# Performance work log

Hardware: AMD Instinct MI355X
Metric: run time of the kernel (lower is better)

The kernel has to match this reference:

```python
import jax, jax.numpy as jnp
import numpy as np

# dims: N sentences, L tokens each, M=2 memory slots/sentence, D hidden, H heads
N, L, M, D, H, FF, V, P, LAYERS = 4, 256, 2, 768, 12, 3072, 32000, 1024, 4
DH = D // H


def setup_inputs() -> dict:
    key = jax.random.key(0)
    ks = jax.random.split(key, 20)
    s = 0.02
    inp = {
        'input_ids': jax.random.randint(ks[0], (N, L), 0, V),
        'memory': jax.random.normal(ks[1], (N, M, D), jnp.float32),
        'emb_table': jax.random.normal(ks[2], (V, D), jnp.float32) * s,
        'pos_table': jax.random.normal(ks[3], (P + 2, D), jnp.float32) * s,
        'Wq': jax.random.normal(ks[4], (LAYERS, D, D), jnp.float32) * s,
        'bq': jnp.zeros((LAYERS, D), jnp.float32),
        'Wk': jax.random.normal(ks[5], (LAYERS, D, D), jnp.float32) * s,
        'bk': jnp.zeros((LAYERS, D), jnp.float32),
        'Wv': jax.random.normal(ks[6], (LAYERS, D, D), jnp.float32) * s,
        'bv': jnp.zeros((LAYERS, D), jnp.float32),
        'W1': jax.random.normal(ks[7], (LAYERS, D, FF), jnp.float32) * s,
        'b1': jnp.zeros((LAYERS, FF), jnp.float32),
        'W2': jax.random.normal(ks[8], (LAYERS, FF, D), jnp.float32) * s,
        'b2': jnp.zeros((LAYERS, D), jnp.float32),
        'g1': jnp.ones((LAYERS, D), jnp.float32),
        'be1': jnp.zeros((LAYERS, D), jnp.float32),
        'g2': jnp.ones((LAYERS, D), jnp.float32),
        'be2': jnp.zeros((LAYERS, D), jnp.float32),
    }
    return inp


def _layer_norm(x, g, b):
    mu = jnp.mean(x, axis=-1, keepdims=True)
    var = jnp.mean((x - mu) ** 2, axis=-1, keepdims=True)
    return (x - mu) / jnp.sqrt(var + 1e-5) * g + b


def _encoder(input_ids, memory, emb_table, pos_table, Wq, bq, Wk, bk, Wv, bv,
             W1, b1, W2, b2, g1, be1, g2, be2):
    base = N * M            # token rows start here in the packed input
    T = base + N * L        # total rows (memory rows + token rows)
    Kk = M + L              # keys per query (own memory + own tokens)

    # position embeddings: memory rows get pos (p % M); tokens get id_pos + M
    mem_pos = jnp.tile(jnp.arange(M), N)                    # (N*M,)
    mem = memory.reshape(N * M, D) + pos_table[mem_pos]
    fwd_pos = jnp.tile(jnp.arange(L) + M, N)                # (N*L,)
    tok = emb_table[input_ids.reshape(-1)] + pos_table[fwd_pos]
    x = jnp.concatenate([mem, tok], axis=0)                 # (T, D)

    # per-sentence key set: its M memory rows then its L token rows
    key_pos = jnp.concatenate([
        jnp.arange(N)[:, None] * M + jnp.arange(M)[None, :],
        base + jnp.arange(N)[:, None] * L + jnp.arange(L)[None, :],
    ], axis=1)                                              # (N, Kk)
    sent = jnp.concatenate([jnp.repeat(jnp.arange(N), M),
                            jnp.repeat(jnp.arange(N), L)])  # (T,)
    gidx = key_pos[sent]                                    # (T, Kk)
    # equal-length sentences => the additive mask built by the torch code is
    # all zeros (key_len == max_key_len for every row), so it is omitted.

    scale = 1.0 / np.sqrt(DH)
    for i in range(LAYERS):
        # K/V are linear row-wise, so project once on all rows then gather
        # (identical math to projecting the gathered tgt, without T-fold GEMM)
        q = (x @ Wq[i] + bq[i]).reshape(T, H, DH)
        kf = (x @ Wk[i] + bk[i]).reshape(T, H, DH)
        vf = (x @ Wv[i] + bv[i]).reshape(T, H, DH)
        kg = kf[gidx]                                       # (T, Kk, H, DH)
        vg = vf[gidx]
        scores = jnp.einsum('thd,tkhd->thk', q, kg) * scale
        probs = jax.nn.softmax(scores, axis=-1)
        ctx = jnp.einsum('thk,tkhd->thd', probs, vg).reshape(T, D)
        x = _layer_norm(x + ctx, g1[i], be1[i])
        h = jax.nn.gelu(x @ W1[i] + b1[i], approximate=False)
        x = _layer_norm(x + h @ W2[i] + b2[i], g2[i], be2[i])

    ret = key_pos[:, M:]                                    # (N, L) token rows
    return x[ret]                                           # (N, L, D)


def reference(input_ids, memory, emb_table, pos_table, Wq, bq, Wk, bk, Wv, bv,
              W1, b1, W2, b2, g1, be1, g2, be2):
    return _encoder(input_ids, memory, emb_table, pos_table, Wq, bq, Wk, bk,
                    Wv, bv, W1, b1, W2, b2, g1, be1, g2, be2)
```

## Files before the change

kernel.cpp:

```cpp
#include <hip/hip_runtime.h>
#include <hip/hip_bf16.h>
#include <math.h>

#define N_      4
#define L_      256
#define M_      2
#define D_      768
#define H_      12
#define FF_     3072
#define DH_     64
#define LAYERS_ 4
#define BASE_   8
#define T_      1032
#define TP_     1088
#define KK_     258
#define QS_     2304
#define PS_     264

typedef __bf16 bf16x8 __attribute__((ext_vector_type(8)));
typedef float  f32x4  __attribute__((ext_vector_type(4)));

__device__ __forceinline__ void async_load16(const __hip_bfloat16* g, __hip_bfloat16* l) {
  __builtin_amdgcn_global_load_lds(
      (const __attribute__((address_space(1))) unsigned int*)g,
      (__attribute__((address_space(3))) unsigned int*)l, 16, 0, 0);
}

__global__ __launch_bounds__(256) void transpose_cast_kernel(
    const float* __restrict__ src, __hip_bfloat16* __restrict__ dst, int K, int N) {
  __shared__ float tile[32][33];
  const int k0 = blockIdx.y * 32, n0 = blockIdx.x * 32;
  const int r = threadIdx.x >> 5, c = threadIdx.x & 31;
  #pragma unroll
  for (int i = 0; i < 4; ++i)
    tile[r + i * 8][c] = src[(size_t)(k0 + r + i * 8) * N + n0 + c];
  __syncthreads();
  #pragma unroll
  for (int i = 0; i < 4; ++i)
    dst[(size_t)(n0 + r + i * 8) * K + k0 + c] = __float2bfloat16(tile[c][r + i * 8]);
}

__global__ __launch_bounds__(256) void pack_bias_kernel(
    const float* __restrict__ bq, const float* __restrict__ bk,
    const float* __restrict__ bv, float* __restrict__ out) {
  int i = blockIdx.x * 256 + threadIdx.x;
  int l = i / QS_, j = i - l * QS_;
  float v;
  if (j < D_)            v = bq[l * D_ + j];
  else if (j < 2 * D_)   v = bk[l * D_ + (j - D_)];
  else                   v = bv[l * D_ + (j - 2 * D_)];
  out[i] = v;
}

__global__ __launch_bounds__(256) void embed_kernel(
    const int* __restrict__ ids, const float* __restrict__ memory,
    const float* __restrict__ emb, const float* __restrict__ pos,
    float* __restrict__ x, __hip_bfloat16* __restrict__ xb) {
  int row = blockIdx.x;
  const float *src, *p;
  if (row < BASE_) {
    src = memory + (long long)row * D_;
    p   = pos + (row & 1) * D_;
  } else {
    int i = row - BASE_;
    int tok = ids[i];
    src = emb + (long long)tok * D_;
    p   = pos + (M_ + (i & (L_ - 1))) * D_;
  }
  for (int d = threadIdx.x; d < D_; d += 256) {
    float v = src[d] + p[d];
    x[(long long)row * D_ + d]  = v;
    xb[(long long)row * D_ + d] = __float2bfloat16(v);
  }
}

template <int ACT, int WF32, int WBF16, int WVT>
__global__ __launch_bounds__(256) void gemm_mfma(
    const __hip_bfloat16* __restrict__ A,
    const __hip_bfloat16* __restrict__ Bt,
    const float* __restrict__ bias,
    float* __restrict__ C,
    __hip_bfloat16* __restrict__ Cb,
    __hip_bfloat16* __restrict__ vt,
    int N, int K) {
  __shared__ __align__(16) __hip_bfloat16 As[4][64][32];
  __shared__ __align__(16) __hip_bfloat16 Bs[4][64][32];
  const int tid  = threadIdx.x;
  const int lane = tid & 63, wid = tid >> 6;
  const int ln   = lane & 15, qd = lane >> 4;
  const int wm   = wid >> 1, wn = wid & 1;

  const size_t arow = (size_t)(blockIdx.y * 64 + wid * 16 + (lane >> 2)) * K + (lane & 3) * 8;
  const size_t brow = (size_t)(blockIdx.x * 64 + wid * 16 + (lane >> 2)) * K + (lane & 3) * 8;

  f32x4 acc[2][2] = {};
  for (int k0 = 0; k0 < K; k0 += 128) {
    #pragma unroll
    for (int s = 0; s < 4; ++s) {
      async_load16(A  + arow + k0 + s * 32, &As[s][wid * 16][0]);
      async_load16(Bt + brow + k0 + s * 32, &Bs[s][wid * 16][0]);
    }
    __syncthreads();
    #pragma unroll
    for (int s = 0; s < 4; ++s) {
      bf16x8 a0 = *(const bf16x8*)&As[s][wm * 32 + ln][qd * 8];
      bf16x8 a1 = *(const bf16x8*)&As[s][wm * 32 + 16 + ln][qd * 8];
      bf16x8 b0 = *(const bf16x8*)&Bs[s][wn * 32 + ln][qd * 8];
      bf16x8 b1 = *(const bf16x8*)&Bs[s][wn * 32 + 16 + ln][qd * 8];
      acc[0][0] = __builtin_amdgcn_mfma_f32_16x16x32_bf16(a0, b0, acc[0][0], 0, 0, 0);
      acc[0][1] = __builtin_amdgcn_mfma_f32_16x16x32_bf16(a0, b1, acc[0][1], 0, 0, 0);
      acc[1][0] = __builtin_amdgcn_mfma_f32_16x16x32_bf16(a1, b0, acc[1][0], 0, 0, 0);
      acc[1][1] = __builtin_amdgcn_mfma_f32_16x16x32_bf16(a1, b1, acc[1][1], 0, 0, 0);
    }
    __syncthreads();
  }
  #pragma unroll
  for (int mt = 0; mt < 2; ++mt) {
    #pragma unroll
    for (int nt = 0; nt < 2; ++nt) {
      const int col = blockIdx.x * 64 + wn * 32 + nt * 16 + ln;
      const float bv = bias[col];
      #pragma unroll
      for (int i = 0; i < 4; ++i) {
        const int row = blockIdx.y * 64 + wm * 32 + mt * 16 + qd * 4 + i;
        float v = acc[mt][nt][i] + bv;
        if (ACT) v = 0.5f * v * (1.f + erff(v * 0.70710678118654752f));
        if (WF32)  C[(size_t)row * N + col]  = v;
        if (WVT) {
          if (col < 2 * D_) Cb[(size_t)row * N + col] = __float2bfloat16(v);
          else              vt[(size_t)(col - 2 * D_) * TP_ + row] = __float2bfloat16(v);
        } else if (WBF16) {
          Cb[(size_t)row * N + col] = __float2bfloat16(v);
        }
      }
    }
  }
}

__global__ __launch_bounds__(256) void attn_mfma(
    const __hip_bfloat16* __restrict__ qkv,
    const __hip_bfloat16* __restrict__ vtb,
    float* __restrict__ ctx) {
  __shared__ __align__(16) __hip_bfloat16 Ps[64][PS_];
  const int qt = blockIdx.x, h = blockIdx.y, b = blockIdx.z;
  const int tid = threadIdx.x;
  const int w = tid >> 6, lane = tid & 63, ln = lane & 15, qd = lane >> 4;

  bf16x8 aq0, aq1;
  {
    int j = qt * 64 + w * 16 + ln;
    int tok = (j < 256) ? (BASE_ + b * L_ + j)
            : ((j < KK_) ? (b * M_ + (j - 256)) : (b * M_));
    const __hip_bfloat16* qp = qkv + (size_t)tok * QS_ + h * DH_ + qd * 8;
    aq0 = *(const bf16x8*)qp;
    aq1 = *(const bf16x8*)(qp + 32);
  }

  f32x4 sa[17];
  #pragma unroll
  for (int nt = 0; nt < 17; ++nt) sa[nt] = (f32x4){0.f, 0.f, 0.f, 0.f};
  #pragma unroll
  for (int nt = 0; nt < 17; ++nt) {
    int key = nt * 16 + ln;
    int ktok = (key < 256) ? (BASE_ + b * L_ + key)
             : ((key < KK_) ? (b * M_ + (key - 256)) : (b * M_));
    const __hip_bfloat16* kp = qkv + (size_t)ktok * QS_ + D_ + h * DH_ + qd * 8;
    bf16x8 b0 = *(const bf16x8*)kp;
    bf16x8 b1 = *(const bf16x8*)(kp + 32);
    sa[nt] = __builtin_amdgcn_mfma_f32_16x16x32_bf16(aq0, b0, sa[nt], 0, 0, 0);
    sa[nt] = __builtin_amdgcn_mfma_f32_16x16x32_bf16(aq1, b1, sa[nt], 0, 0, 0);
  }

  #pragma unroll
  for (int i = 0; i < 4; ++i) {
    float v[17];
    #pragma unroll
    for (int nt = 0; nt < 17; ++nt) v[nt] = sa[nt][i] * 0.125f;
    float mx = -1e30f;
    #pragma unroll
    for (int nt = 0; nt < 16; ++nt) mx = fmaxf(mx, v[nt]);
    if (ln < 2) mx = fmaxf(mx, v[16]);
    #pragma unroll
    for (int m = 1; m < 16; m <<= 1) mx = fmaxf(mx, __shfl_xor(mx, m));
    float sum = 0.f;
    #pragma unroll
    for (int nt = 0; nt < 17; ++nt) {
      float e = (nt == 16 && ln >= 2) ? 0.f : __expf(v[nt] - mx);
      v[nt] = e;
      sum += e;
    }
    #pragma unroll
    for (int m = 1; m < 16; m <<= 1) sum += __shfl_xor(sum, m);
    float is = 1.f / sum;
    const int row = w * 16 + qd * 4 + i;
    #pragma unroll
    for (int nt = 0; nt < 17; ++nt)
      if (nt < 16 || ln < 2)
        Ps[row][nt * 16 + ln] = __float2bfloat16(v[nt] * is);
  }

  f32x4 oa[4] = {};
  #pragma unroll
  for (int k0 = 0; k0 < 8; ++k0) {
    bf16x8 ap = *(const bf16x8*)&Ps[w * 16 + ln][k0 * 32 + qd * 8];
    #pragma unroll
    for (int nt = 0; nt < 4; ++nt) {
      const __hip_bfloat16* vp = vtb + (size_t)(h * DH_ + nt * 16 + ln) * TP_
                               + BASE_ + b * L_ + k0 * 32 + qd * 8;
      bf16x8 bv = *(const bf16x8*)vp;
      oa[nt] = __builtin_amdgcn_mfma_f32_16x16x32_bf16(ap, bv, oa[nt], 0, 0, 0);
    }
  }
  {
    float p0[4], p1[4];
    #pragma unroll
    for (int i = 0; i < 4; ++i) {
      p0[i] = __bfloat162float(Ps[w * 16 + qd * 4 + i][256]);
      p1[i] = __bfloat162float(Ps[w * 16 + qd * 4 + i][257]);
    }
    #pragma unroll
    for (int nt = 0; nt < 4; ++nt) {
      const __hip_bfloat16* vp = vtb + (size_t)(h * DH_ + nt * 16 + ln) * TP_ + b * M_;
      float v0 = __bfloat162float(vp[0]);
      float v1 = __bfloat162float(vp[1]);
      #pragma unroll
      for (int i = 0; i < 4; ++i) oa[nt][i] += p0[i] * v0 + p1[i] * v1;
    }
  }

  #pragma unroll
  for (int i = 0; i < 4; ++i) {
    int j = qt * 64 + w * 16 + qd * 4 + i;
    if (j < KK_) {
      int tok = (j < 256) ? (BASE_ + b * L_ + j) : (b * M_ + (j - 256));
      #pragma unroll
      for (int nt = 0; nt < 4; ++nt)
        ctx[(size_t)tok * D_ + h * DH_ + nt * 16 + ln] = oa[nt][i];
    }
  }
}

__global__ __launch_bounds__(256) void add_ln_kernel(
    float* __restrict__ x, const float* __restrict__ delta,
    const float* __restrict__ g, const float* __restrict__ b,
    __hip_bfloat16* __restrict__ xb) {
  __shared__ float sred[4];
  __shared__ float sbc;
  const int t = blockIdx.x, tid = threadIdx.x;
  float y[3];
  float s = 0.f;
  #pragma unroll
  for (int i = 0; i < 3; ++i) {
    int d = tid + i * 256;
    y[i] = x[(long long)t * D_ + d] + delta[(long long)t * D_ + d];
    s += y[i];
  }
  #pragma unroll
  for (int o = 32; o > 0; o >>= 1) s += __shfl_down(s, o);
  if ((tid & 63) == 0) sred[tid >> 6] = s;
  __syncthreads();
  if (tid == 0) sbc = (sred[0] + sred[1] + sred[2] + sred[3]) * (1.f / D_);
  __syncthreads();
  const float mu = sbc;
  __syncthreads();
  float vs = 0.f;
  #pragma unroll
  for (int i = 0; i < 3; ++i) { float d = y[i] - mu; vs += d * d; }
  #pragma unroll
  for (int o = 32; o > 0; o >>= 1) vs += __shfl_down(vs, o);
  if ((tid & 63) == 0) sred[tid >> 6] = vs;
  __syncthreads();
  if (tid == 0) sbc = (sred[0] + sred[1] + sred[2] + sred[3]) * (1.f / D_);
  __syncthreads();
  const float inv = rsqrtf(sbc + 1e-5f);
  #pragma unroll
  for (int i = 0; i < 3; ++i) {
    int d = tid + i * 256;
    float v = (y[i] - mu) * inv * g[d] + b[d];
    x[(long long)t * D_ + d]  = v;
    xb[(long long)t * D_ + d] = __float2bfloat16(v);
  }
}

__global__ __launch_bounds__(256) void out_copy_kernel(
    const float* __restrict__ x, float* __restrict__ out, int n) {
  int i = blockIdx.x * 256 + threadIdx.x;
  if (i < n) out[i] = x[BASE_ * D_ + i];
}

extern "C" void kernel_launch(void* const* d_in, const int* in_sizes, int n_in,
                              void* d_out, int out_size, void* d_ws, size_t ws_size,
                              hipStream_t stream) {
  const int*   ids    = (const int*)  d_in[0];
  const float* memory = (const float*)d_in[1];
  const float* emb    = (const float*)d_in[2];
  const float* pos    = (const float*)d_in[3];
  const float* Wq     = (const float*)d_in[4];
  const float* bq     = (const float*)d_in[5];
  const float* Wk     = (const float*)d_in[6];
  const float* bk     = (const float*)d_in[7];
  const float* Wv     = (const float*)d_in[8];
  const float* bv     = (const float*)d_in[9];
  const float* W1     = (const float*)d_in[10];
  const float* b1     = (const float*)d_in[11];
  const float* W2     = (const float*)d_in[12];
  const float* b2     = (const float*)d_in[13];
  const float* g1     = (const float*)d_in[14];
  const float* be1    = (const float*)d_in[15];
  const float* g2     = (const float*)d_in[16];
  const float* be2    = (const float*)d_in[17];

  char* w = (char*)d_ws;
  float* x    = (float*)w;                      w += (size_t)TP_ * D_ * 4;
  float* cb   = (float*)w;                      w += (size_t)TP_ * D_ * 4;
  float* bqkv = (float*)w;                      w += (size_t)LAYERS_ * QS_ * 4;
  __hip_bfloat16* xb    = (__hip_bfloat16*)w;   w += (size_t)TP_ * D_ * 2;
  __hip_bfloat16* qkvb  = (__hip_bfloat16*)w;   w += (size_t)TP_ * QS_ * 2;
  __hip_bfloat16* vtb   = (__hip_bfloat16*)w;   w += (size_t)D_ * TP_ * 2;
  __hip_bfloat16* hbb   = (__hip_bfloat16*)w;   w += (size_t)TP_ * FF_ * 2;
  __hip_bfloat16* Wqkvt = (__hip_bfloat16*)w;   w += (size_t)LAYERS_ * QS_ * D_ * 2;
  __hip_bfloat16* W1t   = (__hip_bfloat16*)w;   w += (size_t)LAYERS_ * FF_ * D_ * 2;
  __hip_bfloat16* W2t   = (__hip_bfloat16*)w;   w += (size_t)LAYERS_ * D_ * FF_ * 2;

  for (int i = 0; i < LAYERS_; ++i) {
    const size_t wo  = (size_t)i * D_ * D_;
    const size_t wo1 = (size_t)i * D_ * FF_;
    __hip_bfloat16* dqkv = Wqkvt + (size_t)i * QS_ * D_;
    transpose_cast_kernel<<<dim3(D_ / 32, D_ / 32), 256, 0, stream>>>(Wq + wo, dqkv,                       D_, D_);
    transpose_cast_kernel<<<dim3(D_ / 32, D_ / 32), 256, 0, stream>>>(Wk + wo, dqkv + (size_t)D_ * D_,     D_, D_);
    transpose_cast_kernel<<<dim3(D_ / 32, D_ / 32), 256, 0, stream>>>(Wv + wo, dqkv + (size_t)2 * D_ * D_, D_, D_);
    transpose_cast_kernel<<<dim3(FF_ / 32, D_ / 32), 256, 0, stream>>>(W1 + wo1, W1t + (size_t)i * FF_ * D_, D_, FF_);
    transpose_cast_kernel<<<dim3(D_ / 32, FF_ / 32), 256, 0, stream>>>(W2 + wo1, W2t + (size_t)i * D_ * FF_, FF_, D_);
  }
  pack_bias_kernel<<<LAYERS_ * QS_ / 256, 256, 0, stream>>>(bq, bk, bv, bqkv);

  embed_kernel<<<T_, 256, 0, stream>>>(ids, memory, emb, pos, x, xb);

  for (int i = 0; i < LAYERS_; ++i) {
    gemm_mfma<0, 0, 1, 1><<<dim3(QS_ / 64, TP_ / 64), 256, 0, stream>>>(
        xb, Wqkvt + (size_t)i * QS_ * D_, bqkv + i * QS_, nullptr, qkvb, vtb, QS_, D_);
    attn_mfma<<<dim3(5, H_, N_), 256, 0, stream>>>(qkvb, vtb, cb);
    add_ln_kernel<<<T_, 256, 0, stream>>>(x, cb, g1 + i * D_, be1 + i * D_, xb);
    gemm_mfma<1, 0, 1, 0><<<dim3(FF_ / 64, TP_ / 64), 256, 0, stream>>>(
        xb, W1t + (size_t)i * FF_ * D_, b1 + i * FF_, nullptr, hbb, nullptr, FF_, D_);
    gemm_mfma<0, 1, 0, 0><<<dim3(D_ / 64, TP_ / 64), 256, 0, stream>>>(
        hbb, W2t + (size_t)i * D_ * FF_, b2 + i * D_, cb, nullptr, nullptr, D_, FF_);
    add_ln_kernel<<<T_, 256, 0, stream>>>(x, cb, g2 + i * D_, be2 + i * D_, xb);
  }

  out_copy_kernel<<<(out_size + 255) / 256, 256, 0, stream>>>(x, (float*)d_out, out_size);
}
```

Baseline: 596.3 us.

## Use 128x128 double-buffered swizzled MFMA GEMM with split-K for FFN down-projection

```diff
diff --git a/kernel.cpp b/kernel.cpp
--- a/kernel.cpp
+++ b/kernel.cpp
@@ -12,7 +12,7 @@
 #define LAYERS_ 4
 #define BASE_   8
 #define T_      1032
-#define TP_     1088
+#define TP_     1152
 #define KK_     258
 #define QS_     2304
 #define PS_     264
@@ -74,58 +74,90 @@
   }
 }
 
-template <int ACT, int WF32, int WBF16, int WVT>
-__global__ __launch_bounds__(256) void gemm_mfma(
+template <int ACT, int WF32, int WBF16, int WVT, int KL>
+__global__ __launch_bounds__(256) void gemm_mfma128(
     const __hip_bfloat16* __restrict__ A,
     const __hip_bfloat16* __restrict__ Bt,
     const float* __restrict__ bias,
     float* __restrict__ C,
     __hip_bfloat16* __restrict__ Cb,
     __hip_bfloat16* __restrict__ vt,
-    int N, int K) {
-  __shared__ __align__(16) __hip_bfloat16 As[4][64][32];
-  __shared__ __align__(16) __hip_bfloat16 Bs[4][64][32];
+    int N, int lda) {
+  __shared__ __align__(16) __hip_bfloat16 As[2][128 * 64];
+  __shared__ __align__(16) __hip_bfloat16 Bs[2][128 * 64];
   const int tid  = threadIdx.x;
   const int lane = tid & 63, wid = tid >> 6;
   const int ln   = lane & 15, qd = lane >> 4;
   const int wm   = wid >> 1, wn = wid & 1;
-
-  const size_t arow = (size_t)(blockIdx.y * 64 + wid * 16 + (lane >> 2)) * K + (lane & 3) * 8;
-  const size_t brow = (size_t)(blockIdx.x * 64 + wid * 16 + (lane >> 2)) * K + (lane & 3) * 8;
-
-  f32x4 acc[2][2] = {};
-  for (int k0 = 0; k0 < K; k0 += 128) {
-    #pragma unroll
-    for (int s = 0; s < 4; ++s) {
-      async_load16(A  + arow + k0 + s * 32, &As[s][wid * 16][0]);
-      async_load16(Bt + brow + k0 + s * 32, &Bs[s][wid * 16][0]);
-    }
+  const int r8   = lane >> 3;
+  const int c8   = (lane & 7) ^ r8;
+
+  const size_t koff = (size_t)blockIdx.z * KL;
+  const __hip_bfloat16* Ab = A  + ((size_t)blockIdx.y * 128 + wid * 8 + r8) * lda + koff + c8 * 8;
+  const __hip_bfloat16* Bb = Bt + ((size_t)blockIdx.x * 128 + wid * 8 + r8) * lda + koff + c8 * 8;
+
+  f32x4 acc[4][4] = {};
+
+#define STAGE(buf, t) do {                                                    \
+    const size_t kb_ = (size_t)(t) * 64;                                      \
+    _Pragma("unroll")                                                         \
+    for (int s_ = 0; s_ < 4; ++s_) {                                          \
+      async_load16(Ab + (size_t)s_ * 32 * lda + kb_, &As[buf][(s_ * 32 + wid * 8) * 64]); \
+      async_load16(Bb + (size_t)s_ * 32 * lda + kb_, &Bs[buf][(s_ * 32 + wid * 8) * 64]); \
+    }                                                                         \
+  } while (0)
+
+#define COMPUTE(buf) do {                                                     \
+    _Pragma("unroll")                                                         \
+    for (int kk_ = 0; kk_ < 2; ++kk_) {                                       \
+      bf16x8 af_[4], bf_[4];                                                  \
+      _Pragma("unroll")                                                       \
+      for (int m_ = 0; m_ < 4; ++m_) {                                        \
+        int r_ = wm * 64 + m_ * 16 + ln;                                      \
+        af_[m_] = *(const bf16x8*)&As[buf][r_ * 64 + ((kk_ * 4 + qd) ^ (r_ & 7)) * 8]; \
+      }                                                                       \
+      _Pragma("unroll")                                                       \
+      for (int n_ = 0; n_ < 4; ++n_) {                                        \
+        int r_ = wn * 64 + n_ * 16 + ln;                                      \
+        bf_[n_] = *(const bf16x8*)&Bs[buf][r_ * 64 + ((kk_ * 4 + qd) ^ (r_ & 7)) * 8]; \
+      }                                                                       \
+      _Pragma("unroll")                                                       \
+      for (int m_ = 0; m_ < 4; ++m_)                                          \
+        _Pragma("unroll")                                                     \
+        for (int n_ = 0; n_ < 4; ++n_)                                        \
+          acc[m_][n_] = __builtin_amdgcn_mfma_f32_16x16x32_bf16(af_[m_], bf_[n_], acc[m_][n_], 0, 0, 0); \
+    }                                                                         \
+  } while (0)
+
+  constexpr int NT = KL / 64;
+  STAGE(0, 0);
+  __syncthreads();
+  for (int t = 0; t < NT; t += 2) {
+    if (t + 1 < NT) STAGE(1, t + 1);
+    COMPUTE(0);
     __syncthreads();
-    #pragma unroll
-    for (int s = 0; s < 4; ++s) {
-      bf16x8 a0 = *(const bf16x8*)&As[s][wm * 32 + ln][qd * 8];
-      bf16x8 a1 = *(const bf16x8*)&As[s][wm * 32 + 16 + ln][qd * 8];
-      bf16x8 b0 = *(const bf16x8*)&Bs[s][wn * 32 + ln][qd * 8];
-      bf16x8 b1 = *(const bf16x8*)&Bs[s][wn * 32 + 16 + ln][qd * 8];
-      acc[0][0] = __builtin_amdgcn_mfma_f32_16x16x32_bf16(a0, b0, acc[0][0], 0, 0, 0);
-      acc[0][1] = __builtin_amdgcn_mfma_f32_16x16x32_bf16(a0, b1, acc[0][1], 0, 0, 0);
-      acc[1][0] = __builtin_amdgcn_mfma_f32_16x16x32_bf16(a1, b0, acc[1][0], 0, 0, 0);
-      acc[1][1] = __builtin_amdgcn_mfma_f32_16x16x32_bf16(a1, b1, acc[1][1], 0, 0, 0);
-    }
-    __syncthreads();
-  }
-  #pragma unroll
-  for (int mt = 0; mt < 2; ++mt) {
-    #pragma unroll
-    for (int nt = 0; nt < 2; ++nt) {
-      const int col = blockIdx.x * 64 + wn * 32 + nt * 16 + ln;
-      const float bv = bias[col];
+    if (t + 1 < NT) {
+      if (t + 2 < NT) STAGE(0, t + 2);
+      COMPUTE(1);
+      __syncthreads();
+    }
+  }
+#undef STAGE
+#undef COMPUTE
+
+  #pragma unroll
+  for (int mt = 0; mt < 4; ++mt) {
+    #pragma unroll
+    for (int nt = 0; nt < 4; ++nt) {
+      const int col = blockIdx.x * 128 + wn * 64 + nt * 16 + ln;
+      const float bv = (blockIdx.z == 0) ? bias[col] : 0.f;
       #pragma unroll
       for (int i = 0; i < 4; ++i) {
-        const int row = blockIdx.y * 64 + wm * 32 + mt * 16 + qd * 4 + i;
+        const int row = blockIdx.y * 128 + wm * 64 + mt * 16 + qd * 4 + i;
         float v = acc[mt][nt][i] + bv;
         if (ACT) v = 0.5f * v * (1.f + erff(v * 0.70710678118654752f));
-        if (WF32)  C[(size_t)row * N + col]  = v;
+        if (WF32)
+          C[(size_t)blockIdx.z * TP_ * N + (size_t)row * N + col] = v;
         if (WVT) {
           if (col < 2 * D_) Cb[(size_t)row * N + col] = __float2bfloat16(v);
           else              vt[(size_t)(col - 2 * D_) * TP_ + row] = __float2bfloat16(v);
@@ -240,6 +272,7 @@
   }
 }
 
+template <int NS>
 __global__ __launch_bounds__(256) void add_ln_kernel(
     float* __restrict__ x, const float* __restrict__ delta,
     const float* __restrict__ g, const float* __restrict__ b,
@@ -252,8 +285,12 @@
   #pragma unroll
   for (int i = 0; i < 3; ++i) {
     int d = tid + i * 256;
-    y[i] = x[(long long)t * D_ + d] + delta[(long long)t * D_ + d];
-    s += y[i];
+    float v = x[(long long)t * D_ + d];
+    #pragma unroll
+    for (int s2 = 0; s2 < NS; ++s2)
+      v += delta[(size_t)s2 * TP_ * D_ + (long long)t * D_ + d];
+    y[i] = v;
+    s += v;
   }
   #pragma unroll
   for (int o = 32; o > 0; o >>= 1) s += __shfl_down(s, o);
@@ -312,7 +349,7 @@
 
   char* w = (char*)d_ws;
   float* x    = (float*)w;                      w += (size_t)TP_ * D_ * 4;
-  float* cb   = (float*)w;                      w += (size_t)TP_ * D_ * 4;
+  float* cb   = (float*)w;                      w += (size_t)4 * TP_ * D_ * 4;
   float* bqkv = (float*)w;                      w += (size_t)LAYERS_ * QS_ * 4;
   __hip_bfloat16* xb    = (__hip_bfloat16*)w;   w += (size_t)TP_ * D_ * 2;
   __hip_bfloat16* qkvb  = (__hip_bfloat16*)w;   w += (size_t)TP_ * QS_ * 2;
@@ -337,15 +374,15 @@
   embed_kernel<<<T_, 256, 0, stream>>>(ids, memory, emb, pos, x, xb);
 
   for (int i = 0; i < LAYERS_; ++i) {
-    gemm_mfma<0, 0, 1, 1><<<dim3(QS_ / 64, TP_ / 64), 256, 0, stream>>>(
+    gemm_mfma128<0, 0, 1, 1, 768><<<dim3(QS_ / 128, TP_ / 128, 1), 256, 0, stream>>>(
         xb, Wqkvt + (size_t)i * QS_ * D_, bqkv + i * QS_, nullptr, qkvb, vtb, QS_, D_);
     attn_mfma<<<dim3(5, H_, N_), 256, 0, stream>>>(qkvb, vtb, cb);
-    add_ln_kernel<<<T_, 256, 0, stream>>>(x, cb, g1 + i * D_, be1 + i * D_, xb);
-    gemm_mfma<1, 0, 1, 0><<<dim3(FF_ / 64, TP_ / 64), 256, 0, stream>>>(
+    add_ln_kernel<1><<<T_, 256, 0, stream>>>(x, cb, g1 + i * D_, be1 + i * D_, xb);
+    gemm_mfma128<1, 0, 1, 0, 768><<<dim3(FF_ / 128, TP_ / 128, 1), 256, 0, stream>>>(
         xb, W1t + (size_t)i * FF_ * D_, b1 + i * FF_, nullptr, hbb, nullptr, FF_, D_);
-    gemm_mfma<0, 1, 0, 0><<<dim3(D_ / 64, TP_ / 64), 256, 0, stream>>>(
+    gemm_mfma128<0, 1, 0, 0, 768><<<dim3(D_ / 128, TP_ / 128, 4), 256, 0, stream>>>(
         hbb, W2t + (size_t)i * D_ * FF_, b2 + i * D_, cb, nullptr, nullptr, D_, FF_);
-    add_ln_kernel<<<T_, 256, 0, stream>>>(x, cb, g2 + i * D_, be2 + i * D_, xb);
+    add_ln_kernel<4><<<T_, 256, 0, stream>>>(x, cb, g2 + i * D_, be2 + i * D_, xb);
   }
 
   out_copy_kernel<<<(out_size + 255) / 256, 256, 0, stream>>>(x, (float*)d_out, out_size);
```

Measured after the change: 665.6 us. +11.6%, slower.
